# Optimization experiments

Hardware: AMD Instinct MI355X
Metric: run time of the kernel (lower is better)

The kernel has to match this reference:

```python
import jax, jax.numpy as jnp
import numpy as np

KERNEL_MUL = 2.0
KERNEL_NUM = 5


def setup_inputs() -> dict:
    key = jax.random.key(0)
    k1, k2 = jax.random.split(key)
    N, D = 8192, 256
    subggroup = jax.random.randint(k1, (N, 1), 0, 2, dtype=jnp.int64)
    outputs = jax.random.normal(k2, (N, D), dtype=jnp.float32)
    return {"subggroup": subggroup, "outputs": outputs}


def reference(subggroup, outputs):
    # Binary labels: rows with label 0 form `source` (Min), label 1 form `target` (Maj).
    # concat(source, target) is a permutation of `outputs`, so we compute the
    # full NxN multi-RBF kernel once and take masked means -- identical math.
    sub = subggroup[:, 0]
    m0 = (sub == 0).astype(outputs.dtype)  # source mask
    m1 = (sub == 1).astype(outputs.dtype)  # target mask
    n = outputs.shape[0]

    # Pairwise squared L2 distances via matmul (fused cdist), [N, N]
    sq = jnp.sum(outputs * outputs, axis=-1)
    L2 = jnp.maximum(sq[:, None] + sq[None, :] - 2.0 * (outputs @ outputs.T), 0.0)

    # bandwidth computed from detached distances (torch uses L2_distance.data)
    bandwidth = jax.lax.stop_gradient(jnp.sum(L2)) / (n * n - n)
    bandwidth = bandwidth / (KERNEL_MUL ** (KERNEL_NUM // 2))

    K = jnp.zeros_like(L2)
    for i in range(KERNEL_NUM):
        K = K + jnp.exp(-L2 / (bandwidth * (KERNEL_MUL ** i)))

    n0 = jnp.sum(m0)
    n1 = jnp.sum(m1)
    XX = jnp.einsum('i,ij,j->', m0, K, m0) / (n0 * n0)
    YY = jnp.einsum('i,ij,j->', m1, K, m1) / (n1 * n1)
    XY = jnp.einsum('i,ij,j->', m0, K, m1) / (n0 * n1)
    YX = jnp.einsum('i,ij,j->', m1, K, m0) / (n1 * n0)
    return XX + YY - XY - YX
```

## Files before the change

### kernel.cpp

```cpp
#include <hip/hip_runtime.h>

#define N_ROWS 8192
#define DIMS   256
#define NTILE  64
#define NCHUNK 544
#define K1B    256
#define K3B    512

typedef _Float16 f16x4 __attribute__((ext_vector_type(4)));
typedef _Float16 f16x8 __attribute__((ext_vector_type(8)));
typedef float   f32x16 __attribute__((ext_vector_type(16)));

#define WS_PLANE  0
#define WS_SQ     (4 * 1024 * 1024)
#define WS_COLP   (WS_SQ + 32768)
#define WS_SSQ    (WS_COLP + K1B * 256 * 4)
#define WS_N0     (WS_SSQ + K1B * 4)
#define WS_SC     (WS_N0 + K1B * 4)
#define WS_PART   (WS_SC + 64)

struct Scalars {
    unsigned int ctr;
    unsigned int t3;
    float c2;
    float w0;
    float w1;
};

#define BL(dst, p, o) asm volatile("global_load_dwordx4 %0, %1, off offset:" o \
                                   : "=v"(dst) : "v"(p))

__global__ __launch_bounds__(256) void k1_rows(const float* __restrict__ x,
                                               const long long* __restrict__ sub,
                                               float* __restrict__ sq,
                                               float* __restrict__ colpart,
                                               float* __restrict__ ssqpart,
                                               unsigned int* __restrict__ n0part,
                                               unsigned short* __restrict__ plane) {
    __shared__ _Float16 stg[16 * 512];
    __shared__ float cls[4][256];
    __shared__ float smq[4];
    const int t = threadIdx.x;
    const int l = t & 63;
    const int w = t >> 6;
    const int base = blockIdx.x * 32;

    float4 colacc = make_float4(0.f, 0.f, 0.f, 0.f);
    float  my_sumsq = 0.f;

    const int ks  = l >> 2;
    const int shi = ((l >> 1) & 1) * 32;
    const int j4  = (l & 1) * 4;

    #pragma unroll
    for (int r = 0; r < 8; ++r) {
        const int rr  = w * 8 + r;
        const int row = base + rr;
        const float4 v = ((const float4*)(x + (size_t)row * DIMS))[l];
        colacc.x += v.x; colacc.y += v.y; colacc.z += v.z; colacc.w += v.w;

        f16x4 h = { (_Float16)v.x, (_Float16)v.y, (_Float16)v.z, (_Float16)v.w };
        *(f16x4*)&stg[ks * 512 + (rr + shi) * 8 + j4] = h;

        float s = v.x * v.x + v.y * v.y + v.z * v.z + v.w * v.w;
        #pragma unroll
        for (int off = 32; off; off >>= 1) s += __shfl_down(s, off, 64);
        if (l == 0) { sq[row] = s; my_sumsq += s; }
    }
    if (l == 0) smq[w] = my_sumsq;
    *(float4*)&cls[w][l * 4] = colacc;
    __syncthreads();

    {
        const uint4* src = (const uint4*)stg;
        uint4* dst = (uint4*)(plane + (size_t)blockIdx.x * 8192);
        #pragma unroll
        for (int i = 0; i < 4; ++i) dst[i * 256 + t] = src[i * 256 + t];
    }

    colpart[blockIdx.x * 256 + t] = cls[0][t] + cls[1][t] + cls[2][t] + cls[3][t];
    if (t == 0) ssqpart[blockIdx.x] = smq[0] + smq[1] + smq[2] + smq[3];
    if (w == 1) {
        unsigned long long m1 = __ballot(l < 32 && (int)sub[base + l] == 0);
        if (l == 0) n0part[blockIdx.x] = (unsigned int)__popcll(m1);
    }
}

__global__ __launch_bounds__(1024) void k2_scalars(const float* __restrict__ colpart,
                                                   const float* __restrict__ ssqpart,
                                                   const unsigned int* __restrict__ n0part,
                                                   Scalars* sc) {
    __shared__ float cp[4][256];
    __shared__ float r1[16], r2[16], r3[16];
    const int t = threadIdx.x;
    const int l = t & 63;
    const int w = t >> 6;
    const int col = t & 255;
    const int seg = t >> 8;

    float cs = 0.f;
    #pragma unroll 8
    for (int b = seg * 64; b < (seg + 1) * 64; ++b) cs += colpart[b * 256 + col];
    cp[seg][col] = cs;
    const float sv = (t < K1B) ? ssqpart[t] : 0.f;
    const float nv = (t < K1B) ? (float)n0part[t] : 0.f;
    __syncthreads();

    float a1 = 0.f;
    if (t < 256) {
        const float tot = cp[0][t] + cp[1][t] + cp[2][t] + cp[3][t];
        a1 = tot * tot;
    }
    float v1 = a1, v2 = sv, v3 = nv;
    #pragma unroll
    for (int off = 32; off; off >>= 1) {
        v1 += __shfl_down(v1, off, 64);
        v2 += __shfl_down(v2, off, 64);
        v3 += __shfl_down(v3, off, 64);
    }
    if (l == 0) { r1[w] = v1; r2[w] = v2; r3[w] = v3; }
    __syncthreads();
    if (t == 0) {
        double s1 = 0.0, s2 = 0.0, s3 = 0.0;
        #pragma unroll
        for (int i = 0; i < 16; ++i) { s1 += r1[i]; s2 += r2[i]; s3 += r3[i]; }
        const double n = (double)N_ROWS;
        const double sumL2 = 2.0 * n * s2 - 2.0 * s1;
        const double bw = sumL2 / (n * n - n) / 4.0;
        sc->c2 = (float)(-1.4426950408889634 / (16.0 * bw));
        const double n0 = s3;
        const double n1 = n - n0;
        sc->w0 = (float)( 1.0 / n0);
        sc->w1 = (float)(-1.0 / n1);
        sc->ctr = 0u;
        sc->t3  = 0u;
    }
}

__global__ __launch_bounds__(256, 2) void k3_mmd(const unsigned short* __restrict__ plane,
                                                 const long long* __restrict__ sub,
                                                 const float* __restrict__ sq,
                                                 Scalars* sc,
                                                 double* __restrict__ partial,
                                                 float* __restrict__ out) {
    __shared__ char ldsA[65536];
    __shared__ float2 sqwI[128];
    __shared__ double dd[4];
    __shared__ unsigned int qb;

    const int t  = threadIdx.x;
    const int l  = t & 63;
    const int w  = t >> 6;
    const int lh = l >> 5;
    const int ln = l & 31;

    const float c2 = sc->c2, w0 = sc->w0, w1 = sc->w1;

    double dsum = 0.0;
    f16x8 b[16];

    for (;;) {
        __syncthreads();
        if (t == 0) qb = atomicAdd(&sc->ctr, 1u);
        __syncthreads();
        const unsigned q0 = qb;
        if (q0 >= NCHUNK) break;
        int q = (int)q0, bi = 0;
        for (;;) { const int nc = (NTILE - bi + 3) >> 2; if (q < nc) break; q -= nc; ++bi; }
        int bj = bi + q * 4;
        const int ntr = NTILE - bi - q * 4;
        const int nt  = ntr < 4 ? ntr : 4;

        #pragma unroll
        for (int i = 0; i < 16; ++i) {
            const unsigned short* g = plane + (((size_t)(bi * 4 + w) * 16 + i) << 9) + (l << 3);
            char* lp = ldsA + ((w * 16 + i) << 10);
            __builtin_amdgcn_global_load_lds(
                (const __attribute__((address_space(1))) unsigned int*)(const void*)g,
                (__attribute__((address_space(3))) unsigned int*)(void*)lp, 16, 0, 0);
        }
        if (t < 128) {
            const int I = bi * 128 + t;
            sqwI[t] = make_float2(sq[I], ((int)sub[I] == 0) ? w0 : w1);
        }
        {
            const unsigned short* p0 = plane + (((size_t)(bj * 4 + w) * 16) << 9) + (l << 3);
            const unsigned short* p1 = p0 + 2048;
            const unsigned short* p2 = p0 + 4096;
            const unsigned short* p3 = p0 + 6144;
            BL(b[0], p0,"0"); BL(b[1], p0,"1024"); BL(b[2], p0,"2048"); BL(b[3], p0,"3072");
            BL(b[4], p1,"0"); BL(b[5], p1,"1024"); BL(b[6], p1,"2048"); BL(b[7], p1,"3072");
            BL(b[8], p2,"0"); BL(b[9], p2,"1024"); BL(b[10],p2,"2048"); BL(b[11],p2,"3072");
            BL(b[12],p3,"0"); BL(b[13],p3,"1024"); BL(b[14],p3,"2048"); BL(b[15],p3,"3072");
        }
        const int J0 = bj * 128 + w * 32 + ln;
        float sJ  = sq[J0];
        float wJv = ((int)sub[J0] == 0) ? w0 : w1;
        __syncthreads();

        for (int tt = 0; tt < nt; ++tt, ++bj) {
            const bool dg = (bj == bi);
            asm volatile("s_waitcnt vmcnt(0)" ::: "memory");
            __builtin_amdgcn_sched_barrier(0);

            f32x16 acc[4] = {};
            #pragma unroll
            for (int ks = 0; ks < 16; ++ks) {
                #pragma unroll
                for (int m = 0; m < 4; ++m) {
                    const f16x8 a = *(const f16x8*)(ldsA + ((m * 16 + ks) << 10) + (l << 4));
                    acc[m] = __builtin_amdgcn_mfma_f32_32x32x16_f16(a, b[ks], acc[m], 0, 0, 0);
                }
            }

            float sJn = 0.f, wJn = 0.f;
            if (tt + 1 < nt) {
                const unsigned short* p0 = plane + (((size_t)((bj + 1) * 4 + w) * 16) << 9) + (l << 3);
                const unsigned short* p1 = p0 + 2048;
                const unsigned short* p2 = p0 + 4096;
                const unsigned short* p3 = p0 + 6144;
                BL(b[0], p0,"0"); BL(b[1], p0,"1024"); BL(b[2], p0,"2048"); BL(b[3], p0,"3072");
                BL(b[4], p1,"0"); BL(b[5], p1,"1024"); BL(b[6], p1,"2048"); BL(b[7], p1,"3072");
                BL(b[8], p2,"0"); BL(b[9], p2,"1024"); BL(b[10],p2,"2048"); BL(b[11],p2,"3072");
                BL(b[12],p3,"0"); BL(b[13],p3,"1024"); BL(b[14],p3,"2048"); BL(b[15],p3,"3072");
                const int Jn = (bj + 1) * 128 + w * 32 + ln;
                sJn = sq[Jn];
                wJn = ((int)sub[Jn] == 0) ? w0 : w1;
            }

            float part = 0.f;
            #pragma unroll
            for (int m = 0; m < 4; ++m) {
                #pragma unroll
                for (int r = 0; r < 16; ++r) {
                    const int Il = m * 32 + (r & 3) + ((r >> 2) << 3) + (lh << 2);
                    const float2 pi = sqwI[Il];
                    float l2 = fmaxf(pi.x + sJ - 2.f * acc[m][r], 0.f);
                    const float e  = __builtin_amdgcn_exp2f(l2 * c2);
                    const float e2 = e * e, e4 = e2 * e2, e8 = e4 * e4;
                    const float K  = ((e + e2) + (e4 + e8)) + e8 * e8;
                    float w2 = pi.y * wJv;
                    if (dg) {
                        const int Jl = w * 32 + ln;
                        w2 *= (Il < Jl) ? 2.f : ((Il == Jl) ? 1.f : 0.f);
                    }
                    part = fmaf(K, w2, part);
                }
            }
            dsum += (double)part * (dg ? 1.0 : 2.0);
            sJ = sJn; wJv = wJn;
        }
    }

    #pragma unroll
    for (int off = 32; off; off >>= 1) dsum += __shfl_down(dsum, off, 64);
    __syncthreads();
    if (l == 0) dd[w] = dsum;
    __syncthreads();
    if (t == 0) {
        partial[blockIdx.x] = dd[0] + dd[1] + dd[2] + dd[3];
        __threadfence();
        qb = (atomicAdd(&sc->t3, 1u) == K3B - 1) ? 1u : 0u;
    }
    __syncthreads();
    if (qb) {
        __threadfence();
        double v = partial[t] + partial[t + 256];
        #pragma unroll
        for (int off = 32; off; off >>= 1) v += __shfl_down(v, off, 64);
        if (l == 0) dd[w] = v;
        __syncthreads();
        if (t == 0) out[0] = (float)(dd[0] + dd[1] + dd[2] + dd[3]);
    }
}

extern "C" void kernel_launch(void* const* d_in, const int* in_sizes, int n_in,
                              void* d_out, int out_size, void* d_ws, size_t ws_size,
                              hipStream_t stream) {
    const long long* sub = (const long long*)d_in[0];
    const float*     x   = (const float*)d_in[1];
    float* out = (float*)d_out;

    char* ws = (char*)d_ws;
    unsigned short* plane   = (unsigned short*)(ws + WS_PLANE);
    float*          sq      = (float*)(ws + WS_SQ);
    float*          colpart = (float*)(ws + WS_COLP);
    float*          ssqpart = (float*)(ws + WS_SSQ);
    unsigned int*   n0part  = (unsigned int*)(ws + WS_N0);
    Scalars*        sc      = (Scalars*)(ws + WS_SC);
    double*         partial = (double*)(ws + WS_PART);

    k1_rows<<<K1B, 256, 0, stream>>>(x, sub, sq, colpart, ssqpart, n0part, plane);
    k2_scalars<<<1, 1024, 0, stream>>>(colpart, ssqpart, n0part, sc);
    k3_mmd<<<K3B, 256, 0, stream>>>(plane, sub, sq, sc, partial, out);
}
```

Baseline: 127.0 us.

## Remove scalar kernel via atomics and rebalance MMD work chunks to pairs

Removes the single-block k2 reduction kernel. k1 now atomically accumulates column sums, the sum of squares and the label count into a zeroed workspace area, and every k3 block recomputes the bandwidth and the weights itself. The k3 work decomposition also changes from up-to-4-tile chunks to 2-tile chunks plus single-tile leftovers, giving more and smaller chunks for better load balance. This trades a kernel launch and serial reduction for a memset, float atomics with nondeterministic ordering, and more atomic queue traffic in k3.

```diff
diff --git a/kernel.cpp b/kernel.cpp
--- a/kernel.cpp
+++ b/kernel.cpp
@@ -3,7 +3,8 @@
 #define N_ROWS 8192
 #define DIMS   256
 #define NTILE  64
-#define NCHUNK 544
+#define NFULL  1024
+#define NCHUNK 1056
 #define K1B    256
 #define K3B    512
 
@@ -13,18 +14,15 @@
 
 #define WS_PLANE  0
 #define WS_SQ     (4 * 1024 * 1024)
-#define WS_COLP   (WS_SQ + 32768)
-#define WS_SSQ    (WS_COLP + K1B * 256 * 4)
-#define WS_N0     (WS_SSQ + K1B * 4)
-#define WS_SC     (WS_N0 + K1B * 4)
-#define WS_PART   (WS_SC + 64)
+#define WS_RED    (WS_SQ + 32768)
+#define WS_SSQA   (WS_RED + 1024)
+#define WS_N0A    (WS_SSQA + 4)
+#define WS_SC     (WS_N0A + 4)
+#define WS_PART   (WS_RED + 2048)
 
 struct Scalars {
     unsigned int ctr;
     unsigned int t3;
-    float c2;
-    float w0;
-    float w1;
 };
 
 #define BL(dst, p, o) asm volatile("global_load_dwordx4 %0, %1, off offset:" o \
@@ -33,9 +31,9 @@
 __global__ __launch_bounds__(256) void k1_rows(const float* __restrict__ x,
                                                const long long* __restrict__ sub,
                                                float* __restrict__ sq,
-                                               float* __restrict__ colpart,
-                                               float* __restrict__ ssqpart,
-                                               unsigned int* __restrict__ n0part,
+                                               float* __restrict__ colsumA,
+                                               float* __restrict__ ssqA,
+                                               unsigned int* __restrict__ n0A,
                                                unsigned short* __restrict__ plane) {
     __shared__ _Float16 stg[16 * 512];
     __shared__ float cls[4][256];
@@ -78,68 +76,20 @@
         for (int i = 0; i < 4; ++i) dst[i * 256 + t] = src[i * 256 + t];
     }
 
-    colpart[blockIdx.x * 256 + t] = cls[0][t] + cls[1][t] + cls[2][t] + cls[3][t];
-    if (t == 0) ssqpart[blockIdx.x] = smq[0] + smq[1] + smq[2] + smq[3];
+    atomicAdd(&colsumA[t], cls[0][t] + cls[1][t] + cls[2][t] + cls[3][t]);
+    if (t == 0) atomicAdd(ssqA, smq[0] + smq[1] + smq[2] + smq[3]);
     if (w == 1) {
         unsigned long long m1 = __ballot(l < 32 && (int)sub[base + l] == 0);
-        if (l == 0) n0part[blockIdx.x] = (unsigned int)__popcll(m1);
-    }
-}
-
-__global__ __launch_bounds__(1024) void k2_scalars(const float* __restrict__ colpart,
-                                                   const float* __restrict__ ssqpart,
-                                                   const unsigned int* __restrict__ n0part,
-                                                   Scalars* sc) {
-    __shared__ float cp[4][256];
-    __shared__ float r1[16], r2[16], r3[16];
-    const int t = threadIdx.x;
-    const int l = t & 63;
-    const int w = t >> 6;
-    const int col = t & 255;
-    const int seg = t >> 8;
-
-    float cs = 0.f;
-    #pragma unroll 8
-    for (int b = seg * 64; b < (seg + 1) * 64; ++b) cs += colpart[b * 256 + col];
-    cp[seg][col] = cs;
-    const float sv = (t < K1B) ? ssqpart[t] : 0.f;
-    const float nv = (t < K1B) ? (float)n0part[t] : 0.f;
-    __syncthreads();
-
-    float a1 = 0.f;
-    if (t < 256) {
-        const float tot = cp[0][t] + cp[1][t] + cp[2][t] + cp[3][t];
-        a1 = tot * tot;
-    }
-    float v1 = a1, v2 = sv, v3 = nv;
-    #pragma unroll
-    for (int off = 32; off; off >>= 1) {
-        v1 += __shfl_down(v1, off, 64);
-        v2 += __shfl_down(v2, off, 64);
-        v3 += __shfl_down(v3, off, 64);
-    }
-    if (l == 0) { r1[w] = v1; r2[w] = v2; r3[w] = v3; }
-    __syncthreads();
-    if (t == 0) {
-        double s1 = 0.0, s2 = 0.0, s3 = 0.0;
-        #pragma unroll
-        for (int i = 0; i < 16; ++i) { s1 += r1[i]; s2 += r2[i]; s3 += r3[i]; }
-        const double n = (double)N_ROWS;
-        const double sumL2 = 2.0 * n * s2 - 2.0 * s1;
-        const double bw = sumL2 / (n * n - n) / 4.0;
-        sc->c2 = (float)(-1.4426950408889634 / (16.0 * bw));
-        const double n0 = s3;
-        const double n1 = n - n0;
-        sc->w0 = (float)( 1.0 / n0);
-        sc->w1 = (float)(-1.0 / n1);
-        sc->ctr = 0u;
-        sc->t3  = 0u;
+        if (l == 0) atomicAdd(n0A, (unsigned int)__popcll(m1));
     }
 }
 
 __global__ __launch_bounds__(256, 2) void k3_mmd(const unsigned short* __restrict__ plane,
                                                  const long long* __restrict__ sub,
                                                  const float* __restrict__ sq,
+                                                 const float* __restrict__ colsumA,
+                                                 const float* __restrict__ ssqA,
+                                                 const unsigned int* __restrict__ n0A,
                                                  Scalars* sc,
                                                  double* __restrict__ partial,
                                                  float* __restrict__ out) {
@@ -154,7 +104,22 @@
     const int lh = l >> 5;
     const int ln = l & 31;
 
-    const float c2 = sc->c2, w0 = sc->w0, w1 = sc->w1;
+    float c2, w0, w1;
+    {
+        const float4 c4 = ((const float4*)colsumA)[l];
+        float cs2 = c4.x * c4.x + c4.y * c4.y + c4.z * c4.z + c4.w * c4.w;
+        #pragma unroll
+        for (int off = 32; off; off >>= 1) cs2 += __shfl_xor(cs2, off, 64);
+        const float ssq = *ssqA;
+        const float n0f = (float)*n0A;
+        const double n = (double)N_ROWS;
+        const double sumL2 = 2.0 * n * (double)ssq - 2.0 * (double)cs2;
+        const double bw = sumL2 / (n * n - n) / 4.0;
+        c2 = (float)(-1.4426950408889634 / (16.0 * bw));
+        const double n0 = (double)n0f, n1 = n - n0;
+        w0 = (float)( 1.0 / n0);
+        w1 = (float)(-1.0 / n1);
+    }
 
     double dsum = 0.0;
     f16x8 b[16];
@@ -165,11 +130,17 @@
         __syncthreads();
         const unsigned q0 = qb;
         if (q0 >= NCHUNK) break;
-        int q = (int)q0, bi = 0;
-        for (;;) { const int nc = (NTILE - bi + 3) >> 2; if (q < nc) break; q -= nc; ++bi; }
-        int bj = bi + q * 4;
-        const int ntr = NTILE - bi - q * 4;
-        const int nt  = ntr < 4 ? ntr : 4;
+        int bi, bj, nt;
+        if (q0 < NFULL) {
+            int q = (int)q0; bi = 0;
+            while (q >= ((NTILE - bi) >> 1)) { q -= (NTILE - bi) >> 1; ++bi; }
+            bj = bi + q * 2;
+            nt = 2;
+        } else {
+            bi = 2 * (int)(q0 - NFULL) + 1;
+            bj = NTILE - 1;
+            nt = 1;
+        }
 
         #pragma unroll
         for (int i = 0; i < 16; ++i) {
@@ -284,13 +255,13 @@
     char* ws = (char*)d_ws;
     unsigned short* plane   = (unsigned short*)(ws + WS_PLANE);
     float*          sq      = (float*)(ws + WS_SQ);
-    float*          colpart = (float*)(ws + WS_COLP);
-    float*          ssqpart = (float*)(ws + WS_SSQ);
-    unsigned int*   n0part  = (unsigned int*)(ws + WS_N0);
+    float*          colsumA = (float*)(ws + WS_RED);
+    float*          ssqA    = (float*)(ws + WS_SSQA);
+    unsigned int*   n0A     = (unsigned int*)(ws + WS_N0A);
     Scalars*        sc      = (Scalars*)(ws + WS_SC);
     double*         partial = (double*)(ws + WS_PART);
 
-    k1_rows<<<K1B, 256, 0, stream>>>(x, sub, sq, colpart, ssqpart, n0part, plane);
-    k2_scalars<<<1, 1024, 0, stream>>>(colpart, ssqpart, n0part, sc);
-    k3_mmd<<<K3B, 256, 0, stream>>>(plane, sub, sq, sc, partial, out);
+    hipMemsetAsync(ws + WS_RED, 0, 1040, stream);
+    k1_rows<<<K1B, 256, 0, stream>>>(x, sub, sq, colsumA, ssqA, n0A, plane);
+    k3_mmd<<<K3B, 256, 0, stream>>>(plane, sub, sq, colsumA, ssqA, n0A, sc, partial, out);
 }
```

New measurement: 120.0 us. 1.06x faster.
